# Kernel optimization log

Measured on AMD Instinct MI355X. Metric: run time of the kernel, lower is better.

Reference implementation:

```python
import jax, jax.numpy as jnp
import numpy as np

BLANK_INDEX = 0


def setup_inputs() -> dict:
    key = jax.random.key(0)
    k1, k2 = jax.random.split(key)
    T, B, C, L = 128, 128, 8192, 50
    preds = jax.random.normal(k1, (T, B, C), dtype=jnp.float32)
    trans_targets = jax.random.randint(k2, (B, L), 0, C, dtype=jnp.int64)
    return {"preds": preds, "trans_targets": trans_targets}


def reference(preds, trans_targets):
    T, B, C = preds.shape
    # softmax over classes, then mean over time -> [B, C]
    p = jnp.mean(jax.nn.softmax(preds, axis=2), axis=0)

    # per-row class-count histogram (Counter loop in the original).
    # Out-of-range labels (>= C) are dropped by routing them to a dummy bin C.
    valid = trans_targets < C
    idx = jnp.where(valid, trans_targets, C)

    def row_hist(row_idx):  # row_idx: [L] int
        return jnp.zeros((C + 1,), dtype=preds.dtype).at[row_idx].add(1.0)

    counts = jax.vmap(row_hist)(idx)[:, :C]  # [B, C]

    # blank bin overwritten with T - (# of valid positive labels)
    per_target_length = jnp.sum(valid & (trans_targets > 0), axis=1)  # [B]
    counts = counts.at[:, BLANK_INDEX].set(
        jnp.asarray(T, preds.dtype) - per_target_length.astype(preds.dtype))

    batch_targets = counts / jnp.asarray(T, preds.dtype)
    loss = -jnp.sum(jnp.log(p) * batch_targets) / jnp.asarray(B, preds.dtype)
    return loss
```

## Files before the change

### kernel.cpp

```cpp
#include <hip/hip_runtime.h>
#include <math.h>

#define T_DIM 128
#define B_DIM 128
#define C_DIM 8192
#define L_DIM 50
#define SLOTS (L_DIM + 1)

__global__ __launch_bounds__(256) void softmax_acc_kernel(
    const float* __restrict__ preds,
    const int* __restrict__ targets,
    float* __restrict__ acc)
{
    const int tb  = blockIdx.x;
    const int b   = tb & (B_DIM - 1);
    const int tid = threadIdx.x;
    const float* row = preds + (size_t)tb * C_DIM;

    float s = 0.f;
    #pragma unroll
    for (int k = 0; k < 8; ++k) {
        const float4 v = ((const float4*)row)[k * 256 + tid];
        s += __expf(v.x) + __expf(v.y) + __expf(v.z) + __expf(v.w);
    }

    #pragma unroll
    for (int off = 32; off > 0; off >>= 1)
        s += __shfl_xor(s, off, 64);
    __shared__ float reds[4];
    if ((tid & 63) == 0) reds[tid >> 6] = s;
    __syncthreads();
    const float inv_d = 1.0f / (reds[0] + reds[1] + reds[2] + reds[3]);

    if (tid < SLOTS) {
        int c;
        if (tid == 0) {
            c = 0;
        } else {
            const int lab = targets[b * L_DIM + (tid - 1)];
            c = (lab > 0 && lab < C_DIM) ? lab : -1;
        }
        if (c >= 0) {
            const float val = __expf(row[c]) * inv_d;
            atomicAdd(&acc[b * SLOTS + tid], val);
        }
    }
}

__global__ __launch_bounds__(128) void finalize_kernel(
    const int* __restrict__ targets,
    const float* __restrict__ acc,
    float* __restrict__ out)
{
    const int b = threadIdx.x;
    const float invT = 1.0f / (float)T_DIM;
    float loss_b = 0.f;
    int n_valid = 0;
    for (int l = 0; l < L_DIM; ++l) {
        const int lab = targets[b * L_DIM + l];
        if (lab > 0 && lab < C_DIM) {
            ++n_valid;
            loss_b += logf(acc[b * SLOTS + 1 + l] * invT);
        }
    }
    loss_b += (float)(T_DIM - n_valid) * logf(acc[b * SLOTS] * invT);

    #pragma unroll
    for (int off = 32; off > 0; off >>= 1)
        loss_b += __shfl_xor(loss_b, off, 64);
    __shared__ float red[2];
    if ((threadIdx.x & 63) == 0) red[threadIdx.x >> 6] = loss_b;
    __syncthreads();
    if (threadIdx.x == 0)
        out[0] = -(red[0] + red[1]) / ((float)T_DIM * (float)B_DIM);
}

extern "C" void kernel_launch(void* const* d_in, const int* in_sizes, int n_in,
                              void* d_out, int out_size, void* d_ws, size_t ws_size,
                              hipStream_t stream) {
    const float* preds   = (const float*)d_in[0];
    const int*   targets = (const int*)d_in[1];
    float* acc = (float*)d_ws;
    float* out = (float*)d_out;

    hipMemsetAsync(acc, 0, (size_t)B_DIM * SLOTS * sizeof(float), stream);

    softmax_acc_kernel<<<T_DIM * B_DIM, 256, 0, stream>>>(preds, targets, acc);
    finalize_kernel<<<1, B_DIM, 0, stream>>>(targets, acc, out);
}
```

Measured before the change: 692.4 us.

## Replace atomic accumulation with per-timestep prob buffer and two-stage reduction

```diff
diff --git a/kernel.cpp b/kernel.cpp
--- a/kernel.cpp
+++ b/kernel.cpp
@@ -7,10 +7,10 @@
 #define L_DIM 50
 #define SLOTS (L_DIM + 1)
 
-__global__ __launch_bounds__(256) void softmax_acc_kernel(
+__global__ __launch_bounds__(256) void softmax_probs_kernel(
     const float* __restrict__ preds,
     const int* __restrict__ targets,
-    float* __restrict__ acc)
+    float* __restrict__ probs)
 {
     const int tb  = blockIdx.x;
     const int b   = tb & (B_DIM - 1);
@@ -40,38 +40,54 @@
             const int lab = targets[b * L_DIM + (tid - 1)];
             c = (lab > 0 && lab < C_DIM) ? lab : -1;
         }
-        if (c >= 0) {
-            const float val = __expf(row[c]) * inv_d;
-            atomicAdd(&acc[b * SLOTS + tid], val);
-        }
+        if (c >= 0)
+            probs[(size_t)tb * SLOTS + tid] = __expf(row[c]) * inv_d;
     }
 }
 
-__global__ __launch_bounds__(128) void finalize_kernel(
+__global__ __launch_bounds__(64) void per_b_loss_kernel(
     const int* __restrict__ targets,
-    const float* __restrict__ acc,
+    const float* __restrict__ probs,
+    float* __restrict__ lossb)
+{
+    const int b = blockIdx.x;
+    const int s = threadIdx.x;
+
+    int lab = -1;
+    if (s >= 1 && s <= L_DIM) lab = targets[b * L_DIM + (s - 1)];
+    const bool valid = (lab > 0 && lab < C_DIM);
+    const unsigned long long mask = __ballot(valid);
+    const int n_valid = __popcll(mask);
+
+    float loss = 0.f;
+    if (s == 0 || valid) {
+        float ps = 0.f;
+        #pragma unroll 4
+        for (int t = 0; t < T_DIM; ++t)
+            ps += probs[(size_t)(t * B_DIM + b) * SLOTS + s];
+        const float lg = logf(ps * (1.0f / (float)T_DIM));
+        loss = (s == 0) ? (float)(T_DIM - n_valid) * lg : lg;
+    }
+
+    #pragma unroll
+    for (int off = 32; off > 0; off >>= 1)
+        loss += __shfl_xor(loss, off, 64);
+    if (s == 0) lossb[b] = loss;
+}
+
+__global__ __launch_bounds__(128) void final_reduce_kernel(
+    const float* __restrict__ lossb,
     float* __restrict__ out)
 {
     const int b = threadIdx.x;
-    const float invT = 1.0f / (float)T_DIM;
-    float loss_b = 0.f;
-    int n_valid = 0;
-    for (int l = 0; l < L_DIM; ++l) {
-        const int lab = targets[b * L_DIM + l];
-        if (lab > 0 && lab < C_DIM) {
-            ++n_valid;
-            loss_b += logf(acc[b * SLOTS + 1 + l] * invT);
-        }
-    }
-    loss_b += (float)(T_DIM - n_valid) * logf(acc[b * SLOTS] * invT);
-
+    float v = lossb[b];
     #pragma unroll
     for (int off = 32; off > 0; off >>= 1)
-        loss_b += __shfl_xor(loss_b, off, 64);
+        v += __shfl_xor(v, off, 64);
     __shared__ float red[2];
-    if ((threadIdx.x & 63) == 0) red[threadIdx.x >> 6] = loss_b;
+    if ((b & 63) == 0) red[b >> 6] = v;
     __syncthreads();
-    if (threadIdx.x == 0)
+    if (b == 0)
         out[0] = -(red[0] + red[1]) / ((float)T_DIM * (float)B_DIM);
 }
 
@@ -80,11 +96,11 @@
                               hipStream_t stream) {
     const float* preds   = (const float*)d_in[0];
     const int*   targets = (const int*)d_in[1];
-    float* acc = (float*)d_ws;
+    float* probs = (float*)d_ws;
+    float* lossb = probs + (size_t)T_DIM * B_DIM * SLOTS;
     float* out = (float*)d_out;
 
-    hipMemsetAsync(acc, 0, (size_t)B_DIM * SLOTS * sizeof(float), stream);
-
-    softmax_acc_kernel<<<T_DIM * B_DIM, 256, 0, stream>>>(preds, targets, acc);
-    finalize_kernel<<<1, B_DIM, 0, stream>>>(targets, acc, out);
+    softmax_probs_kernel<<<T_DIM * B_DIM, 256, 0, stream>>>(preds, targets, probs);
+    per_b_loss_kernel<<<B_DIM, 64, 0, stream>>>(targets, probs, lossb);
+    final_reduce_kernel<<<1, 128, 0, stream>>>(lossb, out);
 }
```

After: 689.3 us. No clear change (-0.4%).
